# Kernel optimization log

Hardware: AMD Instinct MI355X
Metric: run time of the kernel (lower is better)

## Reference

```python
import jax, jax.numpy as jnp
import numpy as np

N = 40000      # nodes (adj.size(0))
ISIZE = 64     # feature dim
K = 24         # kept kNN neighbors per node after d_cut mask
E = N * K      # learner candidate edges
E_ADJ = N * K  # GCN adjacency edges
OMEGA = 0.9
GAMMA = 2.0
D_CUT = 1.5


def setup_inputs() -> dict:
    key = jax.random.key(0)
    k = jax.random.split(key, 8)
    features = jax.random.normal(k[0], (N, ISIZE), jnp.float32)
    sc = 1.0 / np.sqrt(ISIZE)
    W1 = jax.random.normal(k[1], (ISIZE, ISIZE), jnp.float32) * sc
    b1 = jnp.zeros((ISIZE,), jnp.float32)
    W2 = jax.random.normal(k[2], (ISIZE, ISIZE), jnp.float32) * sc
    b2 = jnp.zeros((ISIZE,), jnp.float32)
    adj_row = jax.random.randint(k[3], (E_ADJ,), 0, N, dtype=jnp.int32)
    adj_col = jax.random.randint(k[4], (E_ADJ,), 0, N, dtype=jnp.int32)
    # kNN-style candidate edges: K neighbors per node, no self loops
    i_idx = jnp.repeat(jnp.arange(N, dtype=jnp.int32), K)
    j_idx = (i_idx + jax.random.randint(k[5], (E,), 1, N, dtype=jnp.int32)) % N
    # precomputed distance prior: s_d = 1/exp(gamma*(d/d_cut)^2)
    dist = jax.random.uniform(k[6], (E,), jnp.float32, 0.1, 2.0)
    s_d = jnp.exp(-GAMMA * (dist / D_CUT) ** 2)
    return {"features": features, "W1": W1, "b1": b1, "W2": W2, "b2": b2,
            "s_d": s_d, "adj_row": adj_row, "adj_col": adj_col,
            "i_idx": i_idx, "j_idx": j_idx}


def _gcn(x, W, b, row, col):
    """PyG GCNConv: symmetric norm with self loops, aggregate src=row into dst=col."""
    xw = x @ W
    deg = 1.0 + jax.ops.segment_sum(jnp.ones((row.shape[0],), jnp.float32), col,
                                    num_segments=N)
    dinv = jax.lax.rsqrt(deg)
    msg = (dinv[row] * dinv[col])[:, None] * xw[row]            # [E_ADJ, ISIZE]
    out = jax.ops.segment_sum(msg, col, num_segments=N)
    return out + (dinv * dinv)[:, None] * xw + b                # self-loop + bias


def reference(features, W1, b1, W2, b2, s_d, adj_row, adj_col, i_idx, j_idx):
    # GCN stack (nlayers=2), ReLU between layers
    h = jax.nn.relu(_gcn(features, W1, b1, adj_row, adj_col))
    h = _gcn(h, W2, b2, adj_row, adj_col)
    # F.normalize(h, p=2, dim=-1)
    h = h / jnp.maximum(jnp.linalg.norm(h, axis=-1, keepdims=True), 1e-12)
    # per-edge cosine scores, clamped at 0, blended with distance prior
    s_val = jnp.sum(h[i_idx] * h[j_idx], axis=-1)               # [E]
    s_val = jax.nn.relu(s_val)
    s_val = OMEGA * s_val + (1.0 - OMEGA) * s_d
    # SparseTensor.to_symmetric(reduce='mean'): average with reverse edge if present
    keys = i_idx * N + j_idx                                    # fits int32 (N=4e4)
    rkeys = j_idx * N + i_idx
    order = jnp.argsort(keys)
    sk = keys[order]
    pos = jnp.clip(jnp.searchsorted(sk, rkeys), 0, E - 1)
    found = sk[pos] == rkeys
    rev = order[pos]
    v_sym = jnp.where(found, 0.5 * (s_val + s_val[rev]), s_val)
    # symmetric COO: original edges + reverse copies (zeroed where reverse existed)
    rows_s = jnp.concatenate([i_idx, j_idx])                    # [2E]
    cols_s = jnp.concatenate([j_idx, i_idx])
    vals_s = jnp.concatenate([v_sym, jnp.where(found, 0.0, v_sym)])
    # normalize_adj_symm: D^{-1/2} S D^{-1/2}
    deg = jax.ops.segment_sum(vals_s, rows_s, num_segments=N)
    dinv = jnp.where(deg > 0, jax.lax.rsqrt(jnp.maximum(deg, 1e-12)), 0.0)
    vals_norm = dinv[rows_s] * vals_s * dinv[cols_s]
    return vals_norm, vals_s
```

## Files before the change

kernel.cpp:

```cpp
#include <hip/hip_runtime.h>

#define N_NODES 40000
#define ISIZE   64
#define KNN     24
#define NE      (N_NODES * KNN)
#define OMEGA   0.9f
#define CAP     64
#define NBUCK   80
#define BCAP    16384
#define JBCAP   16384
#define EPT     8

__device__ __forceinline__ float bf2f(unsigned short s) {
    return __uint_as_float(((unsigned)s) << 16);
}
__device__ __forceinline__ unsigned short f2bf(float f) {
    unsigned u = __float_as_uint(f);
    u += 0x7fffu + ((u >> 16) & 1u);
    return (unsigned short)(u >> 16);
}
__device__ __forceinline__ float bflo(unsigned u) { return __uint_as_float(u << 16); }
__device__ __forceinline__ float bfhi(unsigned u) { return __uint_as_float(u & 0xffff0000u); }
__device__ __forceinline__ unsigned pack2(float lo, float hi) {
    return (unsigned)f2bf(lo) | ((unsigned)f2bf(hi) << 16);
}
__device__ __forceinline__ float dot8(uint4 a, uint4 b) {
    return bflo(a.x) * bflo(b.x) + bfhi(a.x) * bfhi(b.x)
         + bflo(a.y) * bflo(b.y) + bfhi(a.y) * bfhi(b.y)
         + bflo(a.z) * bflo(b.z) + bfhi(a.z) * bfhi(b.z)
         + bflo(a.w) * bflo(b.w) + bfhi(a.w) * bfhi(b.w);
}

__global__ void k_mega1(const float* __restrict__ X, const float* __restrict__ W,
                        unsigned short* __restrict__ Y,
                        const int* __restrict__ row, const int* __restrict__ col,
                        const int* __restrict__ j_idx,
                        int* __restrict__ bcnt, unsigned* __restrict__ bbuf,
                        unsigned* __restrict__ ovf2, int* __restrict__ ovf2_cnt,
                        int* __restrict__ jbcnt, unsigned* __restrict__ jbbuf,
                        unsigned* __restrict__ jovf, int* __restrict__ jovf_cnt,
                        unsigned char* __restrict__ revb) {
    __shared__ float sW[64 * 64];
    __shared__ float sX[32 * 64];
    const int GB  = N_NODES / 32;
    const int NBA = (NE + 256 * EPT - 1) / (256 * EPT);
    int bx = blockIdx.x;
    int tid = threadIdx.x;
    if (bx < GB) {
        int row0 = bx * 32;
        for (int t = tid; t < 1024; t += 256)
            ((float4*)sW)[t] = ((const float4*)W)[t];
        for (int t = tid; t < 512; t += 256)
            ((float4*)sX)[t] = ((const float4*)(X + row0 * 64))[t];
        __syncthreads();
        int cc = tid & 63;
        int rl = tid >> 6;
        for (int r = rl; r < 32; r += 4) {
            float acc = 0.0f;
#pragma unroll
            for (int kk = 0; kk < 64; kk++) acc += sX[r * 64 + kk] * sW[kk * 64 + cc];
            Y[(row0 + r) * 64 + cc] = f2bf(acc);
        }
    } else if (bx < GB + 2 * NBA) {
        int* lcnt  = (int*)sW;
        int* lbase = lcnt + NBUCK;
        int blk = bx - GB;
        bool adj = blk < NBA;
        if (!adj) blk -= NBA;
        for (int b = tid; b < NBUCK; b += 256) lcnt[b] = 0;
        __syncthreads();
        int e0 = blk * (256 * EPT);
        int myslot[EPT]; int myb[EPT]; unsigned myp[EPT];
        for (int k = 0; k < EPT; k++) {
            int e = e0 + k * 256 + tid;
            if (e < NE) {
                int b; unsigned p;
                if (adj) { int r = row[e], c = col[e]; b = c >> 9; p = ((unsigned)r << 16) | (unsigned)c; }
                else     { int j = j_idx[e];           b = j >> 9; p = ((unsigned)(j & 511) << 20) | (unsigned)e; }
                myb[k] = b; myp[k] = p;
                myslot[k] = atomicAdd(&lcnt[b], 1);
            } else myb[k] = -1;
        }
        __syncthreads();
        int* gcnt = adj ? bcnt : jbcnt;
        for (int b = tid; b < NBUCK; b += 256)
            lbase[b] = (lcnt[b] > 0) ? atomicAdd(&gcnt[b], lcnt[b]) : 0;
        __syncthreads();
        unsigned* gbuf = adj ? bbuf : jbbuf;
        unsigned* govf = adj ? ovf2 : jovf;
        int* gocnt = adj ? ovf2_cnt : jovf_cnt;
        for (int k = 0; k < EPT; k++) {
            if (myb[k] < 0) continue;
            int pos = lbase[myb[k]] + myslot[k];
            if (pos < BCAP) gbuf[myb[k] * BCAP + pos] = myp[k];
            else { int p = atomicAdd(gocnt, 1); govf[p] = myp[k]; }
        }
    } else {
        int e = (bx - GB - 2 * NBA) * 256 + tid;
        int i = e / KNN;
        int j = j_idx[e];
        const uint4* jj4 = (const uint4*)(j_idx + j * KNN);
        int rt = 255;
#pragma unroll
        for (int k = 5; k >= 0; k--) {
            uint4 u = jj4[k];
            if ((int)u.w == i) rt = 4 * k + 3;
            if ((int)u.z == i) rt = 4 * k + 2;
            if ((int)u.y == i) rt = 4 * k + 1;
            if ((int)u.x == i) rt = 4 * k + 0;
        }
        revb[e] = (unsigned char)rt;
    }
}

__global__ void k_scatter3(const unsigned* __restrict__ bbuf, const int* __restrict__ bcnt,
                           int* __restrict__ cnt, unsigned short* __restrict__ ebuf,
                           unsigned* __restrict__ ovf, int* __restrict__ ovf_cnt,
                           const unsigned* __restrict__ ovf2, const int* __restrict__ ovf2_cnt) {
    __shared__ int lcnt2[512];
    int b = blockIdx.x;
    int tid = threadIdx.x;
    if (tid < 512) lcnt2[tid] = 0;
    __syncthreads();
    int n = min(bcnt[b], BCAP);
    for (int idx = tid; idx < n; idx += 1024) {
        unsigned p = bbuf[b * BCAP + idx];
        int c = (int)(p & 0xffffu), r = (int)(p >> 16);
        int slot = atomicAdd(&lcnt2[c & 511], 1);
        if (slot < CAP) ebuf[c * CAP + slot] = (unsigned short)r;
        else { int q = atomicAdd(ovf_cnt, 1); ovf[q] = p; }
    }
    int m = ovf2_cnt[0];
    for (int idx = tid; idx < m; idx += 1024) {
        unsigned p = ovf2[idx];
        int c = (int)(p & 0xffffu), r = (int)(p >> 16);
        if ((c >> 9) != b) continue;
        int slot = atomicAdd(&lcnt2[c & 511], 1);
        if (slot < CAP) ebuf[c * CAP + slot] = (unsigned short)r;
        else { int q = atomicAdd(ovf_cnt, 1); ovf[q] = p; }
    }
    __syncthreads();
    if (tid < 512) {
        int node = b * 512 + tid;
        if (node < N_NODES) cnt[node] = lcnt2[tid];
    }
}

__global__ void __launch_bounds__(1024, 1)
k_aggemm1(const uint4* __restrict__ Aq, const float* __restrict__ W2,
          unsigned short* __restrict__ C,
          const int* __restrict__ cnt,
          const unsigned short* __restrict__ ebuf, const float* __restrict__ bias,
          const unsigned* __restrict__ ovf, const int* __restrict__ ovf_cnt) {
    __shared__ float sW[64 * 64];
    __shared__ float sB[32 * 64];
    int tid  = threadIdx.x;
    int lane = tid & 63;
    int half = lane >> 5, sl = lane & 31;
    int nl = (tid >> 6) * 2 + half;
    int n  = blockIdx.x * 32 + nl;

    ((float4*)sW)[tid] = ((const float4*)W2)[tid];

    int deg = cnt[n];
    int bucketed = min(deg, CAP);
    int nb0 = min(bucketed, 32);
    int nb1 = bucketed - nb0;

    int   r0v = 0, r1v = 0;
    float d0v = 0.0f, d1v = 0.0f;
    if (sl < nb0) { r0v = (int)ebuf[n * CAP + sl];      d0v = rsqrtf(1.0f + (float)cnt[r0v]); }
    if (sl < nb1) { r1v = (int)ebuf[n * CAP + 32 + sl]; d1v = rsqrtf(1.0f + (float)cnt[r1v]); }

    int g = sl >> 2;
    int f = sl & 3;

    float a[16];
#pragma unroll
    for (int k = 0; k < 16; k++) a[k] = 0.f;
    int np0 = (nb0 + 7) >> 3;
    int np1 = (nb1 + 7) >> 3;

#pragma unroll 4
    for (int d = 0; d < np0; d++) {
        int   q = 8 * d + g;
        int   r = __shfl(r0v, q, 32);
        float c = __shfl(d0v, q, 32);
        uint4 u0 = Aq[r * 8 + f];
        uint4 u1 = Aq[r * 8 + 4 + f];
        a[0]  += c * bflo(u0.x); a[1]  += c * bfhi(u0.x);
        a[2]  += c * bflo(u0.y); a[3]  += c * bfhi(u0.y);
        a[4]  += c * bflo(u0.z); a[5]  += c * bfhi(u0.z);
        a[6]  += c * bflo(u0.w); a[7]  += c * bfhi(u0.w);
        a[8]  += c * bflo(u1.x); a[9]  += c * bfhi(u1.x);
        a[10] += c * bflo(u1.y); a[11] += c * bfhi(u1.y);
        a[12] += c * bflo(u1.z); a[13] += c * bfhi(u1.z);
        a[14] += c * bflo(u1.w); a[15] += c * bfhi(u1.w);
    }
#pragma unroll 4
    for (int d = 0; d < np1; d++) {
        int   q = 8 * d + g;
        int   r = __shfl(r1v, q, 32);
        float c = __shfl(d1v, q, 32);
        uint4 u0 = Aq[r * 8 + f];
        uint4 u1 = Aq[r * 8 + 4 + f];
        a[0]  += c * bflo(u0.x); a[1]  += c * bfhi(u0.x);
        a[2]  += c * bflo(u0.y); a[3]  += c * bfhi(u0.y);
        a[4]  += c * bflo(u0.z); a[5]  += c * bfhi(u0.z);
        a[6]  += c * bflo(u0.w); a[7]  += c * bfhi(u0.w);
        a[8]  += c * bflo(u1.x); a[9]  += c * bfhi(u1.x);
        a[10] += c * bflo(u1.y); a[11] += c * bfhi(u1.y);
        a[12] += c * bflo(u1.z); a[13] += c * bfhi(u1.z);
        a[14] += c * bflo(u1.w); a[15] += c * bfhi(u1.w);
    }
    if (deg > CAP) {
        int m = ovf_cnt[0];
        for (int k2 = 0; k2 < m; k2++) {
            unsigned p = ovf[k2];
            if ((int)(p & 0xffffu) == n && g == 0) {
                int r = (int)(p >> 16);
                float c = rsqrtf(1.0f + (float)cnt[r]);
                uint4 u0 = Aq[r * 8 + f], u1 = Aq[r * 8 + 4 + f];
                a[0]  += c * bflo(u0.x); a[1]  += c * bfhi(u0.x);
                a[2]  += c * bflo(u0.y); a[3]  += c * bfhi(u0.y);
                a[4]  += c * bflo(u0.z); a[5]  += c * bfhi(u0.z);
                a[6]  += c * bflo(u0.w); a[7]  += c * bfhi(u0.w);
                a[8]  += c * bflo(u1.x); a[9]  += c * bfhi(u1.x);
                a[10] += c * bflo(u1.y); a[11] += c * bfhi(u1.y);
                a[12] += c * bflo(u1.z); a[13] += c * bfhi(u1.z);
                a[14] += c * bflo(u1.w); a[15] += c * bfhi(u1.w);
            }
        }
    }
#pragma unroll
    for (int k = 0; k < 16; k++) {
        a[k] += __shfl_xor(a[k], 4, 32);
        a[k] += __shfl_xor(a[k], 8, 32);
        a[k] += __shfl_xor(a[k], 16, 32);
    }

    float di = rsqrtf(1.0f + (float)deg);
    float dd = di * di;
    uint4 s0 = Aq[n * 8 + f], s1 = Aq[n * 8 + 4 + f];
    float4 bA0 = ((const float4*)bias)[2 * f];
    float4 bA1 = ((const float4*)bias)[2 * f + 1];
    float4 bB0 = ((const float4*)(bias + 32))[2 * f];
    float4 bB1 = ((const float4*)(bias + 32))[2 * f + 1];
    if (g == 0) {
        float* dst = sB + nl * 64 + 8 * f;
        dst[0] = fmaxf(di * a[0]  + dd * bflo(s0.x) + bA0.x, 0.f);
        dst[1] = fmaxf(di * a[1]  + dd * bfhi(s0.x) + bA0.y, 0.f);
        dst[2] = fmaxf(di * a[2]  + dd * bflo(s0.y) + bA0.z, 0.f);
        dst[3] = fmaxf(di * a[3]  + dd * bfhi(s0.y) + bA0.w, 0.f);
        dst[4] = fmaxf(di * a[4]  + dd * bflo(s0.z) + bA1.x, 0.f);
        dst[5] = fmaxf(di * a[5]  + dd * bfhi(s0.z) + bA1.y, 0.f);
        dst[6] = fmaxf(di * a[6]  + dd * bflo(s0.w) + bA1.z, 0.f);
        dst[7] = fmaxf(di * a[7]  + dd * bfhi(s0.w) + bA1.w, 0.f);
        float* dst2 = dst + 32;
        dst2[0] = fmaxf(di * a[8]  + dd * bflo(s1.x) + bB0.x, 0.f);
        dst2[1] = fmaxf(di * a[9]  + dd * bfhi(s1.x) + bB0.y, 0.f);
        dst2[2] = fmaxf(di * a[10] + dd * bflo(s1.y) + bB0.z, 0.f);
        dst2[3] = fmaxf(di * a[11] + dd * bfhi(s1.y) + bB0.w, 0.f);
        dst2[4] = fmaxf(di * a[12] + dd * bflo(s1.z) + bB1.x, 0.f);
        dst2[5] = fmaxf(di * a[13] + dd * bfhi(s1.z) + bB1.y, 0.f);
        dst2[6] = fmaxf(di * a[14] + dd * bflo(s1.w) + bB1.z, 0.f);
        dst2[7] = fmaxf(di * a[15] + dd * bfhi(s1.w) + bB1.w, 0.f);
    }
    __syncthreads();

    int col = tid & 63;
    int r0  = tid >> 6;
    float acc0 = 0.f, acc1 = 0.f;
#pragma unroll
    for (int kk = 0; kk < 64; kk++) {
        float wv = sW[kk * 64 + col];
        acc0 += sB[r0 * 64 + kk] * wv;
        acc1 += sB[(r0 + 16) * 64 + kk] * wv;
    }
    int na = blockIdx.x * 32 + r0;
    C[na * 64 + col]        = f2bf(acc0);
    C[(na + 16) * 64 + col] = f2bf(acc1);
}

__global__ void k_aggf4(const uint4* __restrict__ Cq, uint4* __restrict__ Hq,
                        const int* __restrict__ cnt,
                        const unsigned short* __restrict__ ebuf, const float* __restrict__ bias,
                        const unsigned* __restrict__ ovf, const int* __restrict__ ovf_cnt) {
    int w = (blockIdx.x * 256 + threadIdx.x) >> 6;
    int lane = threadIdx.x & 63;
    int half = lane >> 5, sl = lane & 31;
    int n = w * 2 + half;
    if (n >= N_NODES) return;
    int deg = cnt[n];
    int bucketed = min(deg, CAP);
    int nb0 = min(bucketed, 32);
    int nb1 = bucketed - nb0;

    int   r0v = 0, r1v = 0;
    float d0v = 0.0f, d1v = 0.0f;
    if (sl < nb0) { r0v = (int)ebuf[n * CAP + sl];      d0v = rsqrtf(1.0f + (float)cnt[r0v]); }
    if (sl < nb1) { r1v = (int)ebuf[n * CAP + 32 + sl]; d1v = rsqrtf(1.0f + (float)cnt[r1v]); }

    int g = sl >> 2;
    int f = sl & 3;

    float a[16];
#pragma unroll
    for (int k = 0; k < 16; k++) a[k] = 0.f;
    int np0 = (nb0 + 7) >> 3;
    int np1 = (nb1 + 7) >> 3;

#pragma unroll 4
    for (int d = 0; d < np0; d++) {
        int   q = 8 * d + g;
        int   r = __shfl(r0v, q, 32);
        float c = __shfl(d0v, q, 32);
        uint4 u0 = Cq[r * 8 + f];
        uint4 u1 = Cq[r * 8 + 4 + f];
        a[0]  += c * bflo(u0.x); a[1]  += c * bfhi(u0.x);
        a[2]  += c * bflo(u0.y); a[3]  += c * bfhi(u0.y);
        a[4]  += c * bflo(u0.z); a[5]  += c * bfhi(u0.z);
        a[6]  += c * bflo(u0.w); a[7]  += c * bfhi(u0.w);
        a[8]  += c * bflo(u1.x); a[9]  += c * bfhi(u1.x);
        a[10] += c * bflo(u1.y); a[11] += c * bfhi(u1.y);
        a[12] += c * bflo(u1.z); a[13] += c * bfhi(u1.z);
        a[14] += c * bflo(u1.w); a[15] += c * bfhi(u1.w);
    }
#pragma unroll 4
    for (int d = 0; d < np1; d++) {
        int   q = 8 * d + g;
        int   r = __shfl(r1v, q, 32);
        float c = __shfl(d1v, q, 32);
        uint4 u0 = Cq[r * 8 + f];
        uint4 u1 = Cq[r * 8 + 4 + f];
        a[0]  += c * bflo(u0.x); a[1]  += c * bfhi(u0.x);
        a[2]  += c * bflo(u0.y); a[3]  += c * bfhi(u0.y);
        a[4]  += c * bflo(u0.z); a[5]  += c * bfhi(u0.z);
        a[6]  += c * bflo(u0.w); a[7]  += c * bfhi(u0.w);
        a[8]  += c * bflo(u1.x); a[9]  += c * bfhi(u1.x);
        a[10] += c * bflo(u1.y); a[11] += c * bfhi(u1.y);
        a[12] += c * bflo(u1.z); a[13] += c * bfhi(u1.z);
        a[14] += c * bflo(u1.w); a[15] += c * bfhi(u1.w);
    }
    if (deg > CAP) {
        int m = ovf_cnt[0];
        for (int k2 = 0; k2 < m; k2++) {
            unsigned p = ovf[k2];
            if ((int)(p & 0xffffu) == n && g == 0) {
                int r = (int)(p >> 16);
                float c = rsqrtf(1.0f + (float)cnt[r]);
                uint4 u0 = Cq[r * 8 + f], u1 = Cq[r * 8 + 4 + f];
                a[0]  += c * bflo(u0.x); a[1]  += c * bfhi(u0.x);
                a[2]  += c * bflo(u0.y); a[3]  += c * bfhi(u0.y);
                a[4]  += c * bflo(u0.z); a[5]  += c * bfhi(u0.z);
                a[6]  += c * bflo(u0.w); a[7]  += c * bfhi(u0.w);
                a[8]  += c * bflo(u1.x); a[9]  += c * bfhi(u1.x);
                a[10] += c * bflo(u1.y); a[11] += c * bfhi(u1.y);
                a[12] += c * bflo(u1.z); a[13] += c * bfhi(u1.z);
                a[14] += c * bflo(u1.w); a[15] += c * bfhi(u1.w);
            }
        }
    }
#pragma unroll
    for (int k = 0; k < 16; k++) {
        a[k] += __shfl_xor(a[k], 4, 32);
        a[k] += __shfl_xor(a[k], 8, 32);
        a[k] += __shfl_xor(a[k], 16, 32);
    }

    float di = rsqrtf(1.0f + (float)deg);
    float dd = di * di;
    uint4 s0 = Cq[n * 8 + f], s1 = Cq[n * 8 + 4 + f];
    float4 bA0 = ((const float4*)bias)[2 * f];
    float4 bA1 = ((const float4*)bias)[2 * f + 1];
    float4 bB0 = ((const float4*)(bias + 32))[2 * f];
    float4 bB1 = ((const float4*)(bias + 32))[2 * f + 1];
    float v[16];
    v[0]  = di * a[0]  + dd * bflo(s0.x) + bA0.x;
    v[1]  = di * a[1]  + dd * bfhi(s0.x) + bA0.y;
    v[2]  = di * a[2]  + dd * bflo(s0.y) + bA0.z;
    v[3]  = di * a[3]  + dd * bfhi(s0.y) + bA0.w;
    v[4]  = di * a[4]  + dd * bflo(s0.z) + bA1.x;
    v[5]  = di * a[5]  + dd * bfhi(s0.z) + bA1.y;
    v[6]  = di * a[6]  + dd * bflo(s0.w) + bA1.z;
    v[7]  = di * a[7]  + dd * bfhi(s0.w) + bA1.w;
    v[8]  = di * a[8]  + dd * bflo(s1.x) + bB0.x;
    v[9]  = di * a[9]  + dd * bfhi(s1.x) + bB0.y;
    v[10] = di * a[10] + dd * bflo(s1.y) + bB0.z;
    v[11] = di * a[11] + dd * bfhi(s1.y) + bB0.w;
    v[12] = di * a[12] + dd * bflo(s1.z) + bB1.x;
    v[13] = di * a[13] + dd * bfhi(s1.z) + bB1.y;
    v[14] = di * a[14] + dd * bflo(s1.w) + bB1.z;
    v[15] = di * a[15] + dd * bfhi(s1.w) + bB1.w;

    float s = 0.f;
#pragma unroll
    for (int k = 0; k < 16; k++) s += v[k] * v[k];
    s += __shfl_xor(s, 1, 32);
    s += __shfl_xor(s, 2, 32);
    float inv = 1.0f / fmaxf(sqrtf(s), 1e-12f);
#pragma unroll
    for (int k = 0; k < 16; k++) v[k] *= inv;
    if (g == 0) {
        Hq[n * 8 + f]     = make_uint4(pack2(v[0], v[1]),  pack2(v[2], v[3]),
                                       pack2(v[4], v[5]),  pack2(v[6], v[7]));
        Hq[n * 8 + 4 + f] = make_uint4(pack2(v[8], v[9]),  pack2(v[10], v[11]),
                                       pack2(v[12], v[13]), pack2(v[14], v[15]));
    }
}

__global__ void k_dotsym(const uint4* __restrict__ Hq,
                         const float* __restrict__ s_d, const int* __restrict__ j_idx,
                         const unsigned char* __restrict__ revb,
                         float* __restrict__ outS) {
    int t = blockIdx.x * 256 + threadIdx.x;
    int e = t >> 1;
    int f = t & 1;
    int i = e / KNN;
    int j = j_idx[e];
    const uint4* Hi = Hq + i * 8 + 4 * f;
    const uint4* Hj = Hq + j * 8 + 4 * f;
    uint4 a0 = Hi[0], a1 = Hi[1], a2 = Hi[2], a3 = Hi[3];
    uint4 b0 = Hj[0], b1 = Hj[1], b2 = Hj[2], b3 = Hj[3];
    float s = dot8(a0, b0) + dot8(a1, b1) + dot8(a2, b2) + dot8(a3, b3);
    s += __shfl_xor(s, 1);
    if (f == 0) {
        float base = OMEGA * fmaxf(s, 0.0f);
        int rt = revb[e];
        float vv, v2;
        if (rt != 255) {
            int rev = j * KNN + rt;
            vv = base + 0.5f * (1.0f - OMEGA) * (s_d[e] + s_d[rev]);
            v2 = 0.0f;
        } else {
            vv = base + (1.0f - OMEGA) * s_d[e];
            v2 = vv;
        }
        outS[e] = vv;
        outS[NE + e] = v2;
    }
}

__global__ void k_jagg(const unsigned* __restrict__ jbbuf, const int* __restrict__ jbcnt,
                       const float* __restrict__ outS, float* __restrict__ dinv2,
                       const unsigned* __restrict__ jovf, const int* __restrict__ jovf_cnt,
                       const int* __restrict__ j_idx) {
    __shared__ float ld[512];
    int b = blockIdx.x;
    int tid = threadIdx.x;
    if (tid < 512) ld[tid] = 0.0f;
    __syncthreads();
    const float* outSv2 = outS + NE;
    int n = min(jbcnt[b], JBCAP);
    for (int idx = tid; idx < n; idx += 1024) {
        unsigned p = jbbuf[b * JBCAP + idx];
        atomicAdd(&ld[p >> 20], outSv2[p & 0xFFFFFu]);
    }
    int m = jovf_cnt[0];
    for (int t2 = tid; t2 < m; t2 += 1024) {
        int e = (int)(jovf[t2] & 0xFFFFFu);
        int j = j_idx[e];
        if ((j >> 9) == b) atomicAdd(&ld[j & 511], outSv2[e]);
    }
    __syncthreads();
    if (tid < 512) {
        int node = b * 512 + tid;
        if (node < N_NODES) {
            float d = ld[tid];
            const float* pp = outS + node * KNN;
#pragma unroll
            for (int qq = 0; qq < KNN; qq++) d += pp[qq];
            dinv2[node] = (d > 0.0f) ? rsqrtf(fmaxf(d, 1e-12f)) : 0.0f;
        }
    }
}

__global__ void k_norm(const float* __restrict__ outS, const float* __restrict__ dinv2,
                       const int* __restrict__ j_idx, float* __restrict__ out) {
    int t = blockIdx.x * 256 + threadIdx.x;
    int r, c;
    if (t < NE) { r = t / KNN; c = j_idx[t]; }
    else        { int e = t - NE; r = j_idx[e]; c = e / KNN; }
    out[t] = dinv2[r] * outS[t] * dinv2[c];
}

extern "C" void kernel_launch(void* const* d_in, const int* in_sizes, int n_in,
                              void* d_out, int out_size, void* d_ws, size_t ws_size,
                              hipStream_t stream) {
    const float* features = (const float*)d_in[0];
    const float* W1       = (const float*)d_in[1];
    const float* b1       = (const float*)d_in[2];
    const float* W2       = (const float*)d_in[3];
    const float* b2       = (const float*)d_in[4];
    const float* s_d      = (const float*)d_in[5];
    const int*   adj_row  = (const int*)d_in[6];
    const int*   adj_col  = (const int*)d_in[7];
    const int*   j_idx    = (const int*)d_in[9];
    float* out = (float*)d_out;

    const int N64 = N_NODES * 64;
    int*   cnt     = (int*)d_ws;
    int*   ovfcnts = cnt + N_NODES;
    int*   bcnt    = ovfcnts + 16;
    int*   jbcnt   = bcnt + NBUCK;
    float* dinv2   = (float*)(jbcnt + NBUCK);
    unsigned short* A   = (unsigned short*)(dinv2 + N_NODES);
    unsigned short* C   = A + N64;
    unsigned short* H   = C + N64;
    unsigned short* ebuf = H + N64;
    unsigned* ovf    = (unsigned*)(ebuf + N_NODES * CAP);
    unsigned char* revb = (unsigned char*)(ovf + NE);
    unsigned* bbuf   = (unsigned*)(revb + NE);
    unsigned* jbbuf  = bbuf + NBUCK * BCAP;
    unsigned* ovf2   = jbbuf + NBUCK * JBCAP;
    unsigned* jovf   = ovf2 + NE;

    size_t zero_bytes = (size_t)(N_NODES + 16 + 2 * NBUCK) * 4;
    hipMemsetAsync(cnt, 0, zero_bytes, stream);

    const int GB = N_NODES / 32;
    const int NBA = (NE + 256 * EPT - 1) / (256 * EPT);
    const int RB = NE / 256;
    k_mega1<<<GB + 2 * NBA + RB, 256, 0, stream>>>(
        features, W1, A, adj_row, adj_col, j_idx,
        bcnt, bbuf, ovf2, ovfcnts + 4, jbcnt, jbbuf, jovf, ovfcnts + 8, revb);

    k_scatter3<<<NBUCK, 1024, 0, stream>>>(bbuf, bcnt, cnt, ebuf,
                                           ovf, ovfcnts, ovf2, ovfcnts + 4);

    k_aggemm1<<<N_NODES / 32, 1024, 0, stream>>>(
        (const uint4*)A, W2, C, cnt, ebuf, b1, ovf, ovfcnts);

    k_aggf4<<<(N_NODES / 2 * 64 + 255) / 256, 256, 0, stream>>>(
        (const uint4*)C, (uint4*)H, cnt, ebuf, b2, ovf, ovfcnts);

    float* outS = out + 2 * NE;
    k_dotsym<<<NE * 2 / 256, 256, 0, stream>>>(
        (const uint4*)H, s_d, j_idx, revb, outS);

    k_jagg<<<NBUCK, 1024, 0, stream>>>(jbbuf, jbcnt, outS, dinv2, jovf, ovfcnts + 8, j_idx);
    k_norm<<<2 * NE / 256, 256, 0, stream>>>(outS, dinv2, j_idx, out);
}
```

Baseline: 235.4 us.

## Pack four nodes per wavefront in GCN gathers and one thread per edge dot

The two GCN aggregation kernels now give each node 16 lanes instead of 32, so a wavefront handles four nodes and the block handles 64 nodes with a doubled shared tile for the fused GEMM. The shared gather logic moves into a helper that processes neighbor lists in 16-wide segments. The edge dot-product kernel drops the two-threads-per-edge split for one thread per edge over the full 64-wide row. Intent is fewer idle lanes for the average degree of about 24 and fewer launched threads, at the cost of more serial loads per lane and a larger shared-memory footprint.

```diff
diff --git a/kernel.cpp b/kernel.cpp
--- a/kernel.cpp
+++ b/kernel.cpp
@@ -29,6 +29,16 @@
          + bflo(a.y) * bflo(b.y) + bfhi(a.y) * bfhi(b.y)
          + bflo(a.z) * bflo(b.z) + bfhi(a.z) * bfhi(b.z)
          + bflo(a.w) * bflo(b.w) + bfhi(a.w) * bfhi(b.w);
+}
+__device__ __forceinline__ void acc16(float* a, uint4 u0, uint4 u1, float c) {
+    a[0]  += c * bflo(u0.x); a[1]  += c * bfhi(u0.x);
+    a[2]  += c * bflo(u0.y); a[3]  += c * bfhi(u0.y);
+    a[4]  += c * bflo(u0.z); a[5]  += c * bfhi(u0.z);
+    a[6]  += c * bflo(u0.w); a[7]  += c * bfhi(u0.w);
+    a[8]  += c * bflo(u1.x); a[9]  += c * bfhi(u1.x);
+    a[10] += c * bflo(u1.y); a[11] += c * bfhi(u1.y);
+    a[12] += c * bflo(u1.z); a[13] += c * bfhi(u1.z);
+    a[14] += c * bflo(u1.w); a[15] += c * bfhi(u1.w);
 }
 
 __global__ void k_mega1(const float* __restrict__ X, const float* __restrict__ W,
@@ -146,6 +156,62 @@
     }
 }
 
+__device__ __forceinline__ void gather16(const uint4* __restrict__ Xq,
+                                         const int* __restrict__ cnt,
+                                         const unsigned short* __restrict__ ebuf,
+                                         const unsigned* __restrict__ ovf,
+                                         const int* __restrict__ ovf_cnt,
+                                         int n, int deg, int g, int f, int ql,
+                                         float* a) {
+    int bucketed = min(deg, CAP);
+    int b0 = min(bucketed, 16);
+    int b1 = min(max(bucketed - 16, 0), 16);
+    int b2 = min(max(bucketed - 32, 0), 16);
+    int b3 = max(bucketed - 48, 0);
+    int base = n * CAP;
+    int   r0v = 0, r1v = 0, r2v = 0, r3v = 0;
+    float d0v = 0.f, d1v = 0.f, d2v = 0.f, d3v = 0.f;
+    if (ql < b0) { r0v = (int)ebuf[base + ql];      d0v = rsqrtf(1.0f + (float)cnt[r0v]); }
+    if (ql < b1) { r1v = (int)ebuf[base + 16 + ql]; d1v = rsqrtf(1.0f + (float)cnt[r1v]); }
+    if (ql < b2) { r2v = (int)ebuf[base + 32 + ql]; d2v = rsqrtf(1.0f + (float)cnt[r2v]); }
+    if (ql < b3) { r3v = (int)ebuf[base + 48 + ql]; d3v = rsqrtf(1.0f + (float)cnt[r3v]); }
+
+#define GSEG(rv, dv, nb)                                            \
+    {   int np = ((nb) + 3) >> 2;                                   \
+        _Pragma("unroll 4")                                         \
+        for (int d = 0; d < np; d++) {                              \
+            int   q = 4 * d + g;                                    \
+            int   r = __shfl(rv, q, 16);                            \
+            float c = __shfl(dv, q, 16);                            \
+            uint4 u0 = Xq[r * 8 + f];                               \
+            uint4 u1 = Xq[r * 8 + 4 + f];                           \
+            acc16(a, u0, u1, c);                                    \
+        }                                                           \
+    }
+    GSEG(r0v, d0v, b0)
+    GSEG(r1v, d1v, b1)
+    GSEG(r2v, d2v, b2)
+    GSEG(r3v, d3v, b3)
+#undef GSEG
+
+    if (deg > CAP) {
+        int m = ovf_cnt[0];
+        for (int k2 = 0; k2 < m; k2++) {
+            unsigned p = ovf[k2];
+            if ((int)(p & 0xffffu) == n && g == 0) {
+                int r = (int)(p >> 16);
+                float c = rsqrtf(1.0f + (float)cnt[r]);
+                acc16(a, Xq[r * 8 + f], Xq[r * 8 + 4 + f], c);
+            }
+        }
+    }
+#pragma unroll
+    for (int k = 0; k < 16; k++) {
+        a[k] += __shfl_xor(a[k], 4, 16);
+        a[k] += __shfl_xor(a[k], 8, 16);
+    }
+}
+
 __global__ void __launch_bounds__(1024, 1)
 k_aggemm1(const uint4* __restrict__ Aq, const float* __restrict__ W2,
           unsigned short* __restrict__ C,
@@ -153,91 +219,21 @@
           const unsigned short* __restrict__ ebuf, const float* __restrict__ bias,
           const unsigned* __restrict__ ovf, const int* __restrict__ ovf_cnt) {
     __shared__ float sW[64 * 64];
-    __shared__ float sB[32 * 64];
+    __shared__ float sB[64 * 64];
     int tid  = threadIdx.x;
     int lane = tid & 63;
-    int half = lane >> 5, sl = lane & 31;
-    int nl = (tid >> 6) * 2 + half;
-    int n  = blockIdx.x * 32 + nl;
+    int ql   = lane & 15;
+    int g = ql >> 2, f = ql & 3;
+    int nl = (tid >> 6) * 4 + (lane >> 4);
+    int n  = blockIdx.x * 64 + nl;
 
     ((float4*)sW)[tid] = ((const float4*)W2)[tid];
 
     int deg = cnt[n];
-    int bucketed = min(deg, CAP);
-    int nb0 = min(bucketed, 32);
-    int nb1 = bucketed - nb0;
-
-    int   r0v = 0, r1v = 0;
-    float d0v = 0.0f, d1v = 0.0f;
-    if (sl < nb0) { r0v = (int)ebuf[n * CAP + sl];      d0v = rsqrtf(1.0f + (float)cnt[r0v]); }
-    if (sl < nb1) { r1v = (int)ebuf[n * CAP + 32 + sl]; d1v = rsqrtf(1.0f + (float)cnt[r1v]); }
-
-    int g = sl >> 2;
-    int f = sl & 3;
-
     float a[16];
 #pragma unroll
     for (int k = 0; k < 16; k++) a[k] = 0.f;
-    int np0 = (nb0 + 7) >> 3;
-    int np1 = (nb1 + 7) >> 3;
-
-#pragma unroll 4
-    for (int d = 0; d < np0; d++) {
-        int   q = 8 * d + g;
-        int   r = __shfl(r0v, q, 32);
-        float c = __shfl(d0v, q, 32);
-        uint4 u0 = Aq[r * 8 + f];
-        uint4 u1 = Aq[r * 8 + 4 + f];
-        a[0]  += c * bflo(u0.x); a[1]  += c * bfhi(u0.x);
-        a[2]  += c * bflo(u0.y); a[3]  += c * bfhi(u0.y);
-        a[4]  += c * bflo(u0.z); a[5]  += c * bfhi(u0.z);
-        a[6]  += c * bflo(u0.w); a[7]  += c * bfhi(u0.w);
-        a[8]  += c * bflo(u1.x); a[9]  += c * bfhi(u1.x);
-        a[10] += c * bflo(u1.y); a[11] += c * bfhi(u1.y);
-        a[12] += c * bflo(u1.z); a[13] += c * bfhi(u1.z);
-        a[14] += c * bflo(u1.w); a[15] += c * bfhi(u1.w);
-    }
-#pragma unroll 4
-    for (int d = 0; d < np1; d++) {
-        int   q = 8 * d + g;
-        int   r = __shfl(r1v, q, 32);
-        float c = __shfl(d1v, q, 32);
-        uint4 u0 = Aq[r * 8 + f];
-        uint4 u1 = Aq[r * 8 + 4 + f];
-        a[0]  += c * bflo(u0.x); a[1]  += c * bfhi(u0.x);
-        a[2]  += c * bflo(u0.y); a[3]  += c * bfhi(u0.y);
-        a[4]  += c * bflo(u0.z); a[5]  += c * bfhi(u0.z);
-        a[6]  += c * bflo(u0.w); a[7]  += c * bfhi(u0.w);
-        a[8]  += c * bflo(u1.x); a[9]  += c * bfhi(u1.x);
-        a[10] += c * bflo(u1.y); a[11] += c * bfhi(u1.y);
-        a[12] += c * bflo(u1.z); a[13] += c * bfhi(u1.z);
-        a[14] += c * bflo(u1.w); a[15] += c * bfhi(u1.w);
-    }
-    if (deg > CAP) {
-        int m = ovf_cnt[0];
-        for (int k2 = 0; k2 < m; k2++) {
-            unsigned p = ovf[k2];
-            if ((int)(p & 0xffffu) == n && g == 0) {
-                int r = (int)(p >> 16);
-                float c = rsqrtf(1.0f + (float)cnt[r]);
-                uint4 u0 = Aq[r * 8 + f], u1 = Aq[r * 8 + 4 + f];
-                a[0]  += c * bflo(u0.x); a[1]  += c * bfhi(u0.x);
-                a[2]  += c * bflo(u0.y); a[3]  += c * bfhi(u0.y);
-                a[4]  += c * bflo(u0.z); a[5]  += c * bfhi(u0.z);
-                a[6]  += c * bflo(u0.w); a[7]  += c * bfhi(u0.w);
-                a[8]  += c * bflo(u1.x); a[9]  += c * bfhi(u1.x);
-                a[10] += c * bflo(u1.y); a[11] += c * bfhi(u1.y);
-                a[12] += c * bflo(u1.z); a[13] += c * bfhi(u1.z);
-                a[14] += c * bflo(u1.w); a[15] += c * bfhi(u1.w);
-            }
-        }
-    }
-#pragma unroll
-    for (int k = 0; k < 16; k++) {
-        a[k] += __shfl_xor(a[k], 4, 32);
-        a[k] += __shfl_xor(a[k], 8, 32);
-        a[k] += __shfl_xor(a[k], 16, 32);
-    }
+    gather16(Aq, cnt, ebuf, ovf, ovf_cnt, n, deg, g, f, ql, a);
 
     float di = rsqrtf(1.0f + (float)deg);
     float dd = di * di;
@@ -270,103 +266,39 @@
 
     int col = tid & 63;
     int r0  = tid >> 6;
-    float acc0 = 0.f, acc1 = 0.f;
+    float acc0 = 0.f, acc1 = 0.f, acc2 = 0.f, acc3 = 0.f;
 #pragma unroll
     for (int kk = 0; kk < 64; kk++) {
         float wv = sW[kk * 64 + col];
         acc0 += sB[r0 * 64 + kk] * wv;
         acc1 += sB[(r0 + 16) * 64 + kk] * wv;
-    }
-    int na = blockIdx.x * 32 + r0;
+        acc2 += sB[(r0 + 32) * 64 + kk] * wv;
+        acc3 += sB[(r0 + 48) * 64 + kk] * wv;
+    }
+    int na = blockIdx.x * 64 + r0;
     C[na * 64 + col]        = f2bf(acc0);
     C[(na + 16) * 64 + col] = f2bf(acc1);
-}
-
-__global__ void k_aggf4(const uint4* __restrict__ Cq, uint4* __restrict__ Hq,
+    C[(na + 32) * 64 + col] = f2bf(acc2);
+    C[(na + 48) * 64 + col] = f2bf(acc3);
+}
+
+__global__ void k_aggf5(const uint4* __restrict__ Cq, uint4* __restrict__ Hq,
                         const int* __restrict__ cnt,
                         const unsigned short* __restrict__ ebuf, const float* __restrict__ bias,
                         const unsigned* __restrict__ ovf, const int* __restrict__ ovf_cnt) {
-    int w = (blockIdx.x * 256 + threadIdx.x) >> 6;
+    int t = blockIdx.x * 256 + threadIdx.x;
+    int w = t >> 6;
     int lane = threadIdx.x & 63;
-    int half = lane >> 5, sl = lane & 31;
-    int n = w * 2 + half;
+    int ql = lane & 15;
+    int g = ql >> 2, f = ql & 3;
+    int n = w * 4 + (lane >> 4);
     if (n >= N_NODES) return;
     int deg = cnt[n];
-    int bucketed = min(deg, CAP);
-    int nb0 = min(bucketed, 32);
-    int nb1 = bucketed - nb0;
-
-    int   r0v = 0, r1v = 0;
-    float d0v = 0.0f, d1v = 0.0f;
-    if (sl < nb0) { r0v = (int)ebuf[n * CAP + sl];      d0v = rsqrtf(1.0f + (float)cnt[r0v]); }
-    if (sl < nb1) { r1v = (int)ebuf[n * CAP + 32 + sl]; d1v = rsqrtf(1.0f + (float)cnt[r1v]); }
-
-    int g = sl >> 2;
-    int f = sl & 3;
 
     float a[16];
 #pragma unroll
     for (int k = 0; k < 16; k++) a[k] = 0.f;
-    int np0 = (nb0 + 7) >> 3;
-    int np1 = (nb1 + 7) >> 3;
-
-#pragma unroll 4
-    for (int d = 0; d < np0; d++) {
-        int   q = 8 * d + g;
-        int   r = __shfl(r0v, q, 32);
-        float c = __shfl(d0v, q, 32);
-        uint4 u0 = Cq[r * 8 + f];
-        uint4 u1 = Cq[r * 8 + 4 + f];
-        a[0]  += c * bflo(u0.x); a[1]  += c * bfhi(u0.x);
-        a[2]  += c * bflo(u0.y); a[3]  += c * bfhi(u0.y);
-        a[4]  += c * bflo(u0.z); a[5]  += c * bfhi(u0.z);
-        a[6]  += c * bflo(u0.w); a[7]  += c * bfhi(u0.w);
-        a[8]  += c * bflo(u1.x); a[9]  += c * bfhi(u1.x);
-        a[10] += c * bflo(u1.y); a[11] += c * bfhi(u1.y);
-        a[12] += c * bflo(u1.z); a[13] += c * bfhi(u1.z);
-        a[14] += c * bflo(u1.w); a[15] += c * bfhi(u1.w);
-    }
-#pragma unroll 4
-    for (int d = 0; d < np1; d++) {
-        int   q = 8 * d + g;
-        int   r = __shfl(r1v, q, 32);
-        float c = __shfl(d1v, q, 32);
-        uint4 u0 = Cq[r * 8 + f];
-        uint4 u1 = Cq[r * 8 + 4 + f];
-        a[0]  += c * bflo(u0.x); a[1]  += c * bfhi(u0.x);
-        a[2]  += c * bflo(u0.y); a[3]  += c * bfhi(u0.y);
-        a[4]  += c * bflo(u0.z); a[5]  += c * bfhi(u0.z);
-        a[6]  += c * bflo(u0.w); a[7]  += c * bfhi(u0.w);
-        a[8]  += c * bflo(u1.x); a[9]  += c * bfhi(u1.x);
-        a[10] += c * bflo(u1.y); a[11] += c * bfhi(u1.y);
-        a[12] += c * bflo(u1.z); a[13] += c * bfhi(u1.z);
-        a[14] += c * bflo(u1.w); a[15] += c * bfhi(u1.w);
-    }
-    if (deg > CAP) {
-        int m = ovf_cnt[0];
-        for (int k2 = 0; k2 < m; k2++) {
-            unsigned p = ovf[k2];
-            if ((int)(p & 0xffffu) == n && g == 0) {
-                int r = (int)(p >> 16);
-                float c = rsqrtf(1.0f + (float)cnt[r]);
-                uint4 u0 = Cq[r * 8 + f], u1 = Cq[r * 8 + 4 + f];
-                a[0]  += c * bflo(u0.x); a[1]  += c * bfhi(u0.x);
-                a[2]  += c * bflo(u0.y); a[3]  += c * bfhi(u0.y);
-                a[4]  += c * bflo(u0.z); a[5]  += c * bfhi(u0.z);
-                a[6]  += c * bflo(u0.w); a[7]  += c * bfhi(u0.w);
-                a[8]  += c * bflo(u1.x); a[9]  += c * bfhi(u1.x);
-                a[10] += c * bflo(u1.y); a[11] += c * bfhi(u1.y);
-                a[12] += c * bflo(u1.z); a[13] += c * bfhi(u1.z);
-                a[14] += c * bflo(u1.w); a[15] += c * bfhi(u1.w);
-            }
-        }
-    }
-#pragma unroll
-    for (int k = 0; k < 16; k++) {
-        a[k] += __shfl_xor(a[k], 4, 32);
-        a[k] += __shfl_xor(a[k], 8, 32);
-        a[k] += __shfl_xor(a[k], 16, 32);
-    }
+    gather16(Cq, cnt, ebuf, ovf, ovf_cnt, n, deg, g, f, ql, a);
 
     float di = rsqrtf(1.0f + (float)deg);
     float dd = di * di;
@@ -396,8 +328,8 @@
     float s = 0.f;
 #pragma unroll
     for (int k = 0; k < 16; k++) s += v[k] * v[k];
-    s += __shfl_xor(s, 1, 32);
-    s += __shfl_xor(s, 2, 32);
+    s += __shfl_xor(s, 1, 16);
+    s += __shfl_xor(s, 2, 16);
     float inv = 1.0f / fmaxf(sqrtf(s), 1e-12f);
 #pragma unroll
     for (int k = 0; k < 16; k++) v[k] *= inv;
@@ -413,32 +345,27 @@
                          const float* __restrict__ s_d, const int* __restrict__ j_idx,
                          const unsigned char* __restrict__ revb,
                          float* __restrict__ outS) {
-    int t = blockIdx.x * 256 + threadIdx.x;
-    int e = t >> 1;
-    int f = t & 1;
+    int e = blockIdx.x * 256 + threadIdx.x;
     int i = e / KNN;
     int j = j_idx[e];
-    const uint4* Hi = Hq + i * 8 + 4 * f;
-    const uint4* Hj = Hq + j * 8 + 4 * f;
-    uint4 a0 = Hi[0], a1 = Hi[1], a2 = Hi[2], a3 = Hi[3];
-    uint4 b0 = Hj[0], b1 = Hj[1], b2 = Hj[2], b3 = Hj[3];
-    float s = dot8(a0, b0) + dot8(a1, b1) + dot8(a2, b2) + dot8(a3, b3);
-    s += __shfl_xor(s, 1);
-    if (f == 0) {
-        float base = OMEGA * fmaxf(s, 0.0f);
-        int rt = revb[e];
-        float vv, v2;
-        if (rt != 255) {
-            int rev = j * KNN + rt;
-            vv = base + 0.5f * (1.0f - OMEGA) * (s_d[e] + s_d[rev]);
-            v2 = 0.0f;
-        } else {
-            vv = base + (1.0f - OMEGA) * s_d[e];
-            v2 = vv;
-        }
-        outS[e] = vv;
-        outS[NE + e] = v2;
-    }
+    const uint4* Hi = Hq + i * 8;
+    const uint4* Hj = Hq + j * 8;
+    float s = 0.f;
+#pragma unroll
+    for (int k = 0; k < 8; k++) s += dot8(Hi[k], Hj[k]);
+    float base = OMEGA * fmaxf(s, 0.0f);
+    int rt = revb[e];
+    float vv, v2;
+    if (rt != 255) {
+        int rev = j * KNN + rt;
+        vv = base + 0.5f * (1.0f - OMEGA) * (s_d[e] + s_d[rev]);
+        v2 = 0.0f;
+    } else {
+        vv = base + (1.0f - OMEGA) * s_d[e];
+        v2 = vv;
+    }
+    outS[e] = vv;
+    outS[NE + e] = v2;
 }
 
 __global__ void k_jagg(const unsigned* __restrict__ jbbuf, const int* __restrict__ jbcnt,
@@ -528,14 +455,14 @@
     k_scatter3<<<NBUCK, 1024, 0, stream>>>(bbuf, bcnt, cnt, ebuf,
                                            ovf, ovfcnts, ovf2, ovfcnts + 4);
 
-    k_aggemm1<<<N_NODES / 32, 1024, 0, stream>>>(
+    k_aggemm1<<<N_NODES / 64, 1024, 0, stream>>>(
         (const uint4*)A, W2, C, cnt, ebuf, b1, ovf, ovfcnts);
 
-    k_aggf4<<<(N_NODES / 2 * 64 + 255) / 256, 256, 0, stream>>>(
+    k_aggf5<<<(N_NODES / 4 * 64 + 255) / 256, 256, 0, stream>>>(
         (const uint4*)C, (uint4*)H, cnt, ebuf, b2, ovf, ovfcnts);
 
     float* outS = out + 2 * NE;
-    k_dotsym<<<NE * 2 / 256, 256, 0, stream>>>(
+    k_dotsym<<<NE / 256, 256, 0, stream>>>(
         (const uint4*)H, s_d, j_idx, revb, outS);
 
     k_jagg<<<NBUCK, 1024, 0, stream>>>(jbbuf, jbcnt, outS, dinv2, jovf, ovfcnts + 8, j_idx);
```

New measurement: 242.3 us. 1.03x slower.
